# Optimization experiments

Hardware: AMD Instinct MI355X
Metric: run time of the kernel (lower is better)

Reference implementation:

```python
import jax, jax.numpy as jnp
import numpy as np

B, T, D, H, UNITS = 32, 2048, 512, 512, 512

def setup_inputs() -> dict:
    key = jax.random.key(0)
    ks = jax.random.split(key, 5)
    scale = 0.02
    return {
        "features": jax.random.normal(ks[0], (B, T, D), dtype=jnp.float32),
        "hidden": jax.random.normal(ks[1], (B, H), dtype=jnp.float32),
        "Wk": jax.random.normal(ks[2], (D, UNITS), dtype=jnp.float32) * scale,
        "Wb": jnp.zeros((UNITS,), dtype=jnp.float32),
        "Uk": jax.random.normal(ks[3], (H, UNITS), dtype=jnp.float32) * scale,
        "Ub": jnp.zeros((UNITS,), dtype=jnp.float32),
        "Vk": jax.random.normal(ks[4], (UNITS, 1), dtype=jnp.float32) * scale,
        "Vb": jnp.zeros((1,), dtype=jnp.float32),
    }

def reference(features, hidden, Wk, Wb, Uk, Ub, Vk, Vb):
    # features: [B, T, D], hidden: [B, H]
    wf = jnp.einsum('btd,du->btu', features, Wk) + Wb          # [B, T, U]
    uh = (hidden @ Uk + Ub)[:, None, :]                        # [B, 1, U]
    score = jnp.tanh(wf + uh)                                  # [B, T, U]
    logits = jnp.einsum('btu,uo->bto', score, Vk) + Vb         # [B, T, 1]
    attention_weights = jax.nn.softmax(logits, axis=1)         # [B, T, 1]
    context_vector = jnp.sum(attention_weights * features, axis=1)  # [B, D]
    return context_vector, attention_weights
```

## Files before the change

### kernel.cpp

```cpp
#include <hip/hip_runtime.h>
#include <stdint.h>


typedef unsigned short ushort_t;
typedef __attribute__((ext_vector_type(8))) short short8;
typedef __attribute__((ext_vector_type(4))) float f32x4;
typedef __attribute__((ext_vector_type(2))) float float2v;
typedef __attribute__((ext_vector_type(2))) __bf16 bf162v;

#define GLOBAL_AS __attribute__((address_space(1)))
#define LDS_AS    __attribute__((address_space(3)))

__device__ __forceinline__ ushort_t f2bf(float f) {
    uint32_t u = __builtin_bit_cast(uint32_t, f);
    u = (u + 0x7fffu + ((u >> 16) & 1u)) >> 16;
    return (ushort_t)u;
}
__device__ __forceinline__ uint32_t pkbf(float a, float b) {
    bf162v r = __builtin_convertvector((float2v){a, b}, bf162v);
    return __builtin_bit_cast(uint32_t, r);
}

__global__ __launch_bounds__(256) void convert_feats(
    const float* __restrict__ f, ushort_t* __restrict__ o)
{
    const size_t i = ((size_t)blockIdx.x * 256 + threadIdx.x) * 8;
    f32x4 a = *(const f32x4*)(f + i);
    f32x4 b = *(const f32x4*)(f + i + 4);
    union { short8 s; uint32_t u[4]; } r;
    r.u[0] = pkbf(a.x, a.y); r.u[1] = pkbf(a.z, a.w);
    r.u[2] = pkbf(b.x, b.y); r.u[3] = pkbf(b.z, b.w);
    *(short8*)(o + i) = r.s;
}

__global__ __launch_bounds__(256) void prep_uh(
    const float* __restrict__ hidden, const float* __restrict__ Uk,
    const float* __restrict__ Ub, const float* __restrict__ Wb,
    float* __restrict__ uh)
{
    const int b  = blockIdx.x >> 3;
    const int u  = (blockIdx.x & 7) * 64 + (threadIdx.x & 63);
    const int k0 = (threadIdx.x >> 6) * 128;
    const float* hr = hidden + b * 512;
    float acc = 0.f;
    #pragma unroll 8
    for (int k = k0; k < k0 + 128; ++k)
        acc += hr[k] * Uk[k * 512 + u];
    __shared__ float red[256];
    red[threadIdx.x] = acc;
    __syncthreads();
    if (threadIdx.x < 64) {
        const int ul = threadIdx.x;
        uh[b * 512 + u] = red[ul] + red[ul + 64] + red[ul + 128] + red[ul + 192]
                        + Ub[u] + Wb[u];
    }
}

__global__ __launch_bounds__(256) void prep_wkt(
    const float* __restrict__ Wk, ushort_t* __restrict__ WkT)
{
    __shared__ float t[32][33];
    const int ti = blockIdx.x >> 4;
    const int tj = blockIdx.x & 15;
    const int tx = threadIdx.x & 31;
    const int ty = threadIdx.x >> 5;
    #pragma unroll
    for (int q = 0; q < 4; ++q) {
        const int r = ty * 4 + q;
        t[r][tx] = Wk[(ti * 32 + r) * 512 + tj * 32 + tx];
    }
    __syncthreads();
    #pragma unroll
    for (int q = 0; q < 4; ++q) {
        const int r = ty * 4 + q;
        WkT[(tj * 32 + r) * 512 + ti * 32 + tx] = f2bf(t[tx][r]);
    }
}

template<bool CONV>
__global__ __launch_bounds__(256) void attn_gemm(
    const float* __restrict__ afp, const ushort_t* __restrict__ abf,
    const ushort_t* __restrict__ WkT, const float* __restrict__ uh,
    const float* __restrict__ Vk, float* __restrict__ lg4)
{
    __shared__ __align__(16) short As[128 * 32];
    __shared__ __align__(16) short Bs[128 * 32];
    __shared__ float uh_s[128];
    __shared__ float vk_s[128];
    __shared__ float lpart[2][128];

    const int tid  = threadIdx.x;
    const int lane = tid & 63;
    const int quad = lane >> 4;
    const int lc   = lane & 15;
    const int wave = tid >> 6;
    const int wm   = wave >> 1;
    const int wn   = wave & 1;
    const int mblk = blockIdx.x >> 2;
    const int nc   = blockIdx.x & 3;
    const int m0   = mblk * 128;
    const int bidx = m0 >> 11;

    if (tid < 128) {
        uh_s[tid] = uh[bidx * 512 + nc * 128 + tid];
        vk_s[tid] = Vk[nc * 128 + tid];
    }

    f32x4 acc[4][4];
    #pragma unroll
    for (int tm = 0; tm < 4; ++tm)
        #pragma unroll
        for (int tn = 0; tn < 4; ++tn)
            acc[tm][tn] = (f32x4){0.f, 0.f, 0.f, 0.f};

    for (int ks = 0; ks < 16; ++ks) {
        const int k0 = ks * 32;
        __syncthreads();
        {
            const int rowB = tid >> 2;
            const int kqB  = (tid & 3) * 8;
            #pragma unroll
            for (int rnd = 0; rnd < 2; ++rnd) {
                const int li  = rnd * 256 + tid;
                const int row = rnd * 64 + rowB;
                const ushort_t* gb = WkT + (size_t)(nc * 128 + row) * 512 + k0 + kqB;
                __builtin_amdgcn_global_load_lds(
                    (const GLOBAL_AS void*)gb, (LDS_AS void*)(Bs + li * 8), 16, 0, 0);
            }
        }
        if constexpr (CONV) {
            const int row = tid >> 1;
            const int k16 = (tid & 1) * 16;
            const float* ga = afp + (size_t)(m0 + row) * 512 + k0 + k16;
            f32x4 a0 = *(const f32x4*)(ga);
            f32x4 a1 = *(const f32x4*)(ga + 4);
            f32x4 a2 = *(const f32x4*)(ga + 8);
            f32x4 a3 = *(const f32x4*)(ga + 12);
            union { short8 s; uint32_t u[4]; } r0, r1;
            r0.u[0] = pkbf(a0.x, a0.y); r0.u[1] = pkbf(a0.z, a0.w);
            r0.u[2] = pkbf(a1.x, a1.y); r0.u[3] = pkbf(a1.z, a1.w);
            r1.u[0] = pkbf(a2.x, a2.y); r1.u[1] = pkbf(a2.z, a2.w);
            r1.u[2] = pkbf(a3.x, a3.y); r1.u[3] = pkbf(a3.z, a3.w);
            *(short8*)(As + row * 32 + k16)     = r0.s;
            *(short8*)(As + row * 32 + k16 + 8) = r1.s;
        } else {
            const int rowA = tid >> 2;
            const int kqA  = (tid & 3) * 8;
            #pragma unroll
            for (int rnd = 0; rnd < 2; ++rnd) {
                const int li  = rnd * 256 + tid;
                const int row = rnd * 64 + rowA;
                const ushort_t* ga = abf + (size_t)(m0 + row) * 512 + k0 + kqA;
                __builtin_amdgcn_global_load_lds(
                    (const GLOBAL_AS void*)ga, (LDS_AS void*)(As + li * 8), 16, 0, 0);
            }
        }
        __syncthreads();

        short8 af[4], bfr[4];
        #pragma unroll
        for (int t4 = 0; t4 < 4; ++t4) {
            af[t4]  = *(const short8*)(As + (wm * 64 + t4 * 16 + lc) * 32 + quad * 8);
            bfr[t4] = *(const short8*)(Bs + (wn * 64 + t4 * 16 + lc) * 32 + quad * 8);
        }
        #pragma unroll
        for (int tm = 0; tm < 4; ++tm)
            #pragma unroll
            for (int tn = 0; tn < 4; ++tn)
                acc[tm][tn] = __builtin_amdgcn_mfma_f32_16x16x32_bf16(
                    af[tm], bfr[tn], acc[tm][tn], 0, 0, 0);
    }

    float rp[16];
    #pragma unroll
    for (int i = 0; i < 16; ++i) rp[i] = 0.f;
    #pragma unroll
    for (int tn = 0; tn < 4; ++tn) {
        const int nl  = wn * 64 + tn * 16 + lc;
        const float uhv = uh_s[nl];
        const float vkv = vk_s[nl];
        #pragma unroll
        for (int tm = 0; tm < 4; ++tm)
            #pragma unroll
            for (int i = 0; i < 4; ++i) {
                const float x = acc[tm][tn][i] + uhv;
                const float e = __expf(2.0f * x);
                rp[tm * 4 + i] += (1.0f - 2.0f / (e + 1.0f)) * vkv;
            }
    }
    #pragma unroll
    for (int i = 0; i < 16; ++i) {
        float v = rp[i];
        v += __shfl_xor(v, 1, 64);
        v += __shfl_xor(v, 2, 64);
        v += __shfl_xor(v, 4, 64);
        v += __shfl_xor(v, 8, 64);
        rp[i] = v;
    }
    if (lc == 0) {
        #pragma unroll
        for (int tm = 0; tm < 4; ++tm)
            #pragma unroll
            for (int i = 0; i < 4; ++i)
                lpart[wn][wm * 64 + tm * 16 + quad * 4 + i] = rp[tm * 4 + i];
    }
    __syncthreads();
    if (tid < 128)
        lg4[(size_t)nc * 65536 + m0 + tid] = lpart[0][tid] + lpart[1][tid];
}

__global__ __launch_bounds__(256) void softmax_k(
    const float* __restrict__ lg4, float* __restrict__ aw_out)
{
    const int b = blockIdx.x, tid = threadIdx.x;
    const float* p = lg4 + b * 2048;
    float v[8];
    #pragma unroll
    for (int i = 0; i < 8; ++i) {
        const int idx = tid + i * 256;
        v[i] = p[idx] + p[idx + 65536] + p[idx + 131072] + p[idx + 196608];
    }
    float mx = -1e30f;
    #pragma unroll
    for (int i = 0; i < 8; ++i) mx = fmaxf(mx, v[i]);
    #pragma unroll
    for (int off = 32; off >= 1; off >>= 1) mx = fmaxf(mx, __shfl_xor(mx, off, 64));
    __shared__ float redm[4], reds[4];
    const int wv = tid >> 6, ln = tid & 63;
    if (ln == 0) redm[wv] = mx;
    __syncthreads();
    mx = fmaxf(fmaxf(redm[0], redm[1]), fmaxf(redm[2], redm[3]));
    float s = 0.f;
    #pragma unroll
    for (int i = 0; i < 8; ++i) { v[i] = __expf(v[i] - mx); s += v[i]; }
    #pragma unroll
    for (int off = 32; off >= 1; off >>= 1) s += __shfl_xor(s, off, 64);
    if (ln == 0) reds[wv] = s;
    __syncthreads();
    s = reds[0] + reds[1] + reds[2] + reds[3];
    const float inv = 1.0f / s;
    #pragma unroll
    for (int i = 0; i < 8; ++i)
        aw_out[b * 2048 + tid + i * 256] = v[i] * inv;
}

__global__ __launch_bounds__(256) void context_k(
    const float* __restrict__ feats, const float* __restrict__ aw,
    float* __restrict__ ctx)
{
    const int b  = blockIdx.x >> 5;
    const int t0 = (blockIdx.x & 31) * 64 + (threadIdx.x >> 7) * 32;
    const int d4 = (threadIdx.x & 127) * 4;
    const float* fp = feats + (size_t)(b * 2048 + t0) * 512 + d4;
    const float* wp = aw + b * 2048 + t0;
    f32x4 a = (f32x4){0.f, 0.f, 0.f, 0.f};
    #pragma unroll 4
    for (int tt = 0; tt < 32; ++tt) {
        const float w = wp[tt];
        const f32x4 f = *(const f32x4*)(fp + (size_t)tt * 512);
        a.x += w * f.x; a.y += w * f.y; a.z += w * f.z; a.w += w * f.w;
    }
    atomicAdd(&ctx[b * 512 + d4],     a.x);
    atomicAdd(&ctx[b * 512 + d4 + 1], a.y);
    atomicAdd(&ctx[b * 512 + d4 + 2], a.z);
    atomicAdd(&ctx[b * 512 + d4 + 3], a.w);
}

__global__ __launch_bounds__(256) void ctx_out_k(
    const float* __restrict__ ctx, float* __restrict__ out)
{
    const int i = blockIdx.x * 256 + threadIdx.x;
    out[i] = ctx[i];
}

extern "C" void kernel_launch(void* const* d_in, const int* in_sizes, int n_in,
                              void* d_out, int out_size, void* d_ws, size_t ws_size,
                              hipStream_t stream)
{
    const float* feats  = (const float*)d_in[0];
    const float* hidden = (const float*)d_in[1];
    const float* Wk     = (const float*)d_in[2];
    const float* Wb     = (const float*)d_in[3];
    const float* Uk     = (const float*)d_in[4];
    const float* Ub     = (const float*)d_in[5];
    const float* Vk     = (const float*)d_in[6];

    float* out       = (float*)d_out;
    float* ctx_out_p = out;
    float* aw_out_p  = out + 16384;

    char* ws = (char*)d_ws;
    float*    uh  = (float*)ws;
    ushort_t* WkT = (ushort_t*)(ws + 65536);
    float*    lg4 = (float*)(ws + 589824);
    float*    ctx = (float*)(ws + 1638400);
    ushort_t* fbf = (ushort_t*)(ws + (2u << 20));

    const bool bigws = ws_size >= ((2ull << 20) + (64ull << 20));

    hipMemsetAsync(ctx, 0, 65536, stream);
    prep_uh  <<<256, 256, 0, stream>>>(hidden, Uk, Ub, Wb, uh);
    prep_wkt <<<256, 256, 0, stream>>>(Wk, WkT);
    if (bigws) {
        convert_feats<<<16384, 256, 0, stream>>>(feats, fbf);
        attn_gemm<false><<<2048, 256, 0, stream>>>(feats, fbf, WkT, uh, Vk, lg4);
    } else {
        attn_gemm<true><<<2048, 256, 0, stream>>>(feats, (const ushort_t*)nullptr,
                                                  WkT, uh, Vk, lg4);
    }
    softmax_k<<<32,   256, 0, stream>>>(lg4, aw_out_p);
    context_k<<<1024, 256, 0, stream>>>(feats, aw_out_p, ctx);
    ctx_out_k<<<64,   256, 0, stream>>>(ctx, ctx_out_p);
}
```

Measured before the change: 312.7 us.

## Read bf16 features in context, fuse prep kernels, drop ctx copy, reorder GEMM blocks

```diff
diff --git a/kernel.cpp b/kernel.cpp
--- a/kernel.cpp
+++ b/kernel.cpp
@@ -15,6 +15,10 @@
     uint32_t u = __builtin_bit_cast(uint32_t, f);
     u = (u + 0x7fffu + ((u >> 16) & 1u)) >> 16;
     return (ushort_t)u;
+}
+__device__ __forceinline__ float bf2f(ushort_t h) {
+    uint32_t u = ((uint32_t)h) << 16;
+    return __builtin_bit_cast(float, u);
 }
 __device__ __forceinline__ uint32_t pkbf(float a, float b) {
     bf162v r = __builtin_convertvector((float2v){a, b}, bf162v);
@@ -33,52 +37,52 @@
     *(short8*)(o + i) = r.s;
 }
 
-__global__ __launch_bounds__(256) void prep_uh(
+__global__ __launch_bounds__(256) void prep_fused(
     const float* __restrict__ hidden, const float* __restrict__ Uk,
     const float* __restrict__ Ub, const float* __restrict__ Wb,
-    float* __restrict__ uh)
-{
-    const int b  = blockIdx.x >> 3;
-    const int u  = (blockIdx.x & 7) * 64 + (threadIdx.x & 63);
-    const int k0 = (threadIdx.x >> 6) * 128;
-    const float* hr = hidden + b * 512;
-    float acc = 0.f;
-    #pragma unroll 8
-    for (int k = k0; k < k0 + 128; ++k)
-        acc += hr[k] * Uk[k * 512 + u];
-    __shared__ float red[256];
-    red[threadIdx.x] = acc;
-    __syncthreads();
-    if (threadIdx.x < 64) {
-        const int ul = threadIdx.x;
-        uh[b * 512 + u] = red[ul] + red[ul + 64] + red[ul + 128] + red[ul + 192]
-                        + Ub[u] + Wb[u];
-    }
-}
-
-__global__ __launch_bounds__(256) void prep_wkt(
-    const float* __restrict__ Wk, ushort_t* __restrict__ WkT)
-{
-    __shared__ float t[32][33];
-    const int ti = blockIdx.x >> 4;
-    const int tj = blockIdx.x & 15;
-    const int tx = threadIdx.x & 31;
-    const int ty = threadIdx.x >> 5;
-    #pragma unroll
-    for (int q = 0; q < 4; ++q) {
-        const int r = ty * 4 + q;
-        t[r][tx] = Wk[(ti * 32 + r) * 512 + tj * 32 + tx];
-    }
-    __syncthreads();
-    #pragma unroll
-    for (int q = 0; q < 4; ++q) {
-        const int r = ty * 4 + q;
-        WkT[(tj * 32 + r) * 512 + ti * 32 + tx] = f2bf(t[tx][r]);
+    const float* __restrict__ Wk,
+    float* __restrict__ uh, ushort_t* __restrict__ WkT)
+{
+    if (blockIdx.x < 256) {
+        const int b  = blockIdx.x >> 3;
+        const int u  = (blockIdx.x & 7) * 64 + (threadIdx.x & 63);
+        const int k0 = (threadIdx.x >> 6) * 128;
+        const float* hr = hidden + b * 512;
+        float acc = 0.f;
+        #pragma unroll 8
+        for (int k = k0; k < k0 + 128; ++k)
+            acc += hr[k] * Uk[k * 512 + u];
+        __shared__ float red[256];
+        red[threadIdx.x] = acc;
+        __syncthreads();
+        if (threadIdx.x < 64) {
+            const int ul = threadIdx.x;
+            uh[b * 512 + u] = red[ul] + red[ul + 64] + red[ul + 128] + red[ul + 192]
+                            + Ub[u] + Wb[u];
+        }
+    } else {
+        __shared__ float t[32][33];
+        const int blk = blockIdx.x - 256;
+        const int ti = blk >> 4;
+        const int tj = blk & 15;
+        const int tx = threadIdx.x & 31;
+        const int ty = threadIdx.x >> 5;
+        #pragma unroll
+        for (int q = 0; q < 4; ++q) {
+            const int r = ty * 4 + q;
+            t[r][tx] = Wk[(ti * 32 + r) * 512 + tj * 32 + tx];
+        }
+        __syncthreads();
+        #pragma unroll
+        for (int q = 0; q < 4; ++q) {
+            const int r = ty * 4 + q;
+            WkT[(tj * 32 + r) * 512 + ti * 32 + tx] = f2bf(t[tx][r]);
+        }
     }
 }
 
 template<bool CONV>
-__global__ __launch_bounds__(256) void attn_gemm(
+__global__ __launch_bounds__(256, 4) void attn_gemm(
     const float* __restrict__ afp, const ushort_t* __restrict__ abf,
     const ushort_t* __restrict__ WkT, const float* __restrict__ uh,
     const float* __restrict__ Vk, float* __restrict__ lg4)
@@ -96,8 +100,8 @@
     const int wave = tid >> 6;
     const int wm   = wave >> 1;
     const int wn   = wave & 1;
-    const int mblk = blockIdx.x >> 2;
-    const int nc   = blockIdx.x & 3;
+    const int nc   = (blockIdx.x >> 8) & 3;
+    const int mblk = (blockIdx.x & 255) | ((blockIdx.x >> 10) << 8);
     const int m0   = mblk * 128;
     const int bidx = m0 >> 11;
 
@@ -244,33 +248,39 @@
         aw_out[b * 2048 + tid + i * 256] = v[i] * inv;
 }
 
+template<bool BF>
 __global__ __launch_bounds__(256) void context_k(
-    const float* __restrict__ feats, const float* __restrict__ aw,
-    float* __restrict__ ctx)
-{
-    const int b  = blockIdx.x >> 5;
-    const int t0 = (blockIdx.x & 31) * 64 + (threadIdx.x >> 7) * 32;
+    const ushort_t* __restrict__ fb, const float* __restrict__ ff,
+    const float* __restrict__ aw, float* __restrict__ ctx_out)
+{
+    const int b  = blockIdx.x >> 4;
+    const int t0 = (blockIdx.x & 15) * 128 + (threadIdx.x >> 7) * 64;
     const int d4 = (threadIdx.x & 127) * 4;
-    const float* fp = feats + (size_t)(b * 2048 + t0) * 512 + d4;
     const float* wp = aw + b * 2048 + t0;
     f32x4 a = (f32x4){0.f, 0.f, 0.f, 0.f};
-    #pragma unroll 4
-    for (int tt = 0; tt < 32; ++tt) {
-        const float w = wp[tt];
-        const f32x4 f = *(const f32x4*)(fp + (size_t)tt * 512);
-        a.x += w * f.x; a.y += w * f.y; a.z += w * f.z; a.w += w * f.w;
-    }
-    atomicAdd(&ctx[b * 512 + d4],     a.x);
-    atomicAdd(&ctx[b * 512 + d4 + 1], a.y);
-    atomicAdd(&ctx[b * 512 + d4 + 2], a.z);
-    atomicAdd(&ctx[b * 512 + d4 + 3], a.w);
-}
-
-__global__ __launch_bounds__(256) void ctx_out_k(
-    const float* __restrict__ ctx, float* __restrict__ out)
-{
-    const int i = blockIdx.x * 256 + threadIdx.x;
-    out[i] = ctx[i];
+    if constexpr (BF) {
+        const ushort_t* fp = fb + (size_t)(b * 2048 + t0) * 512 + d4;
+        #pragma unroll 4
+        for (int tt = 0; tt < 64; ++tt) {
+            const float w = wp[tt];
+            union { uint2 u2; ushort_t h[4]; } r;
+            r.u2 = *(const uint2*)(fp + (size_t)tt * 512);
+            a.x += w * bf2f(r.h[0]); a.y += w * bf2f(r.h[1]);
+            a.z += w * bf2f(r.h[2]); a.w += w * bf2f(r.h[3]);
+        }
+    } else {
+        const float* fp = ff + (size_t)(b * 2048 + t0) * 512 + d4;
+        #pragma unroll 4
+        for (int tt = 0; tt < 64; ++tt) {
+            const float w = wp[tt];
+            const f32x4 f = *(const f32x4*)(fp + (size_t)tt * 512);
+            a.x += w * f.x; a.y += w * f.y; a.z += w * f.z; a.w += w * f.w;
+        }
+    }
+    atomicAdd(&ctx_out[b * 512 + d4],     a.x);
+    atomicAdd(&ctx_out[b * 512 + d4 + 1], a.y);
+    atomicAdd(&ctx_out[b * 512 + d4 + 2], a.z);
+    atomicAdd(&ctx_out[b * 512 + d4 + 3], a.w);
 }
 
 extern "C" void kernel_launch(void* const* d_in, const int* in_sizes, int n_in,
@@ -293,22 +303,22 @@
     float*    uh  = (float*)ws;
     ushort_t* WkT = (ushort_t*)(ws + 65536);
     float*    lg4 = (float*)(ws + 589824);
-    float*    ctx = (float*)(ws + 1638400);
     ushort_t* fbf = (ushort_t*)(ws + (2u << 20));
 
     const bool bigws = ws_size >= ((2ull << 20) + (64ull << 20));
 
-    hipMemsetAsync(ctx, 0, 65536, stream);
-    prep_uh  <<<256, 256, 0, stream>>>(hidden, Uk, Ub, Wb, uh);
-    prep_wkt <<<256, 256, 0, stream>>>(Wk, WkT);
+    hipMemsetAsync(ctx_out_p, 0, 65536, stream);
+    prep_fused<<<512, 256, 0, stream>>>(hidden, Uk, Ub, Wb, Wk, uh, WkT);
     if (bigws) {
         convert_feats<<<16384, 256, 0, stream>>>(feats, fbf);
         attn_gemm<false><<<2048, 256, 0, stream>>>(feats, fbf, WkT, uh, Vk, lg4);
+        softmax_k<<<32,  256, 0, stream>>>(lg4, aw_out_p);
+        context_k<true><<<512, 256, 0, stream>>>(fbf, feats, aw_out_p, ctx_out_p);
     } else {
         attn_gemm<true><<<2048, 256, 0, stream>>>(feats, (const ushort_t*)nullptr,
                                                   WkT, uh, Vk, lg4);
-    }
-    softmax_k<<<32,   256, 0, stream>>>(lg4, aw_out_p);
-    context_k<<<1024, 256, 0, stream>>>(feats, aw_out_p, ctx);
-    ctx_out_k<<<64,   256, 0, stream>>>(ctx, ctx_out_p);
-}
+        softmax_k<<<32,  256, 0, stream>>>(lg4, aw_out_p);
+        context_k<false><<<512, 256, 0, stream>>>((const ushort_t*)nullptr, feats,
+                                                  aw_out_p, ctx_out_p);
+    }
+}
```

Result: faster. 287.5 us (-8.1%).
